# Optimization experiments

Measured on AMD Instinct MI355X. Metric: run time of the kernel, lower is better.

## Reference

```python
import jax, jax.numpy as jnp
import numpy as np

E = 2048        # embed_dim
H = 16          # num_heads
HKV = 4         # num_heads_kv (GQA)
D = 128         # head_dim
DCONV = 4       # causal depthwise conv width
ROT_DIM = 128   # rotary_emb_dim (= head_dim, full rotation)
ROT_BASE = 10000.0
QKV_DIM = D * (H + 2 * HKV)  # 3072
B, S = 2, 2048


def setup_inputs() -> dict:
    key = jax.random.key(0)
    ks = jax.random.split(key, 7)
    return {
        "x": jax.random.normal(ks[0], (B, S, E), jnp.float32),
        "W_in": jax.random.normal(ks[1], (E, QKV_DIM), jnp.float32) * 0.02,
        "b_in": jax.random.normal(ks[2], (QKV_DIM,), jnp.float32) * 0.02,
        "conv_w": jax.random.normal(ks[3], (QKV_DIM, DCONV), jnp.float32) * 0.1,
        "conv_b": jax.random.normal(ks[4], (QKV_DIM,), jnp.float32) * 0.02,
        "W_out": jax.random.normal(ks[5], (E, E), jnp.float32) * 0.02,
        "b_out": jax.random.normal(ks[6], (E,), jnp.float32) * 0.02,
    }


def _rotary_cos_sin(seqlen, dtype):
    # flash_attn RotaryEmbedding: inv_freq over even indices
    inv_freq = 1.0 / (ROT_BASE ** (np.arange(0, ROT_DIM, 2, dtype=np.float32) / ROT_DIM))
    t = np.arange(seqlen, dtype=np.float32)
    freqs = np.outer(t, inv_freq)                      # [S, ROT_DIM/2]
    return jnp.asarray(np.cos(freqs), dtype), jnp.asarray(np.sin(freqs), dtype)


def _apply_rotary(xh, cos, sin):
    # non-interleaved: rotate halves of the first ROT_DIM dims. xh: [B,S,h,D]
    x1 = xh[..., : ROT_DIM // 2]
    x2 = xh[..., ROT_DIM // 2 : ROT_DIM]
    c = cos[None, :, None, :]
    s = sin[None, :, None, :]
    rot = jnp.concatenate([x1 * c - x2 * s, x2 * c + x1 * s], axis=-1)
    return jnp.concatenate([rot, xh[..., ROT_DIM:]], axis=-1)


def _forward(x, W_in, b_in, conv_w, conv_b, W_out, b_out):
    b, s, _ = x.shape
    qkv = x @ W_in + b_in                              # [B,S,QKV_DIM]

    # causal depthwise conv1d (kernel DCONV, left-pad DCONV-1, trim right)
    xp = jnp.pad(qkv, ((0, 0), (DCONV - 1, 0), (0, 0)))
    conv = conv_b
    for k in range(DCONV):
        conv = conv + xp[:, k : k + s, :] * conv_w[:, k]
    qkv = conv                                         # [B,S,QKV_DIM]

    q, kv = jnp.split(qkv, [H * D], axis=-1)
    q = q.reshape(b, s, H, D)
    kv = kv.reshape(b, s, 2, HKV, D)
    k, v = kv[:, :, 0], kv[:, :, 1]                    # [B,S,HKV,D]

    cos, sin = _rotary_cos_sin(s, x.dtype)
    q = _apply_rotary(q, cos, sin)
    k = _apply_rotary(k, cos, sin)

    # GQA: repeat kv heads
    rep = H // HKV
    k = jnp.repeat(k, rep, axis=2)                     # [B,S,H,D]
    v = jnp.repeat(v, rep, axis=2)

    scale = 1.0 / np.sqrt(D)
    scores = jnp.einsum("bqhd,bkhd->bhqk", q, k) * scale
    causal = jnp.tril(jnp.ones((s, s), bool))
    scores = jnp.where(causal[None, None], scores, jnp.finfo(scores.dtype).min)
    probs = jax.nn.softmax(scores, axis=-1)
    ctx = jnp.einsum("bhqk,bkhd->bqhd", probs, v)      # [B,S,H,D]

    return ctx.reshape(b, s, H * D) @ W_out + b_out    # [B,S,E]


def reference(x, W_in, b_in, conv_w, conv_b, W_out, b_out):
    return _forward(x, W_in, b_in, conv_w, conv_b, W_out, b_out)
```

## Files before the change

kernel.cpp:

```cpp
#include <hip/hip_runtime.h>
#include <hip/hip_bf16.h>

#define B_    2
#define S_    2048
#define E_    2048
#define H_    16
#define HKV_  4
#define D_    128
#define QKV_  3072

#define LOG2E  1.4426950408889634f
#define SCALE  0.08838834764831845f
#define SL     0.127517431f
#define DEFER_THR 62.7f

typedef __attribute__((ext_vector_type(8))) short short8;
typedef __attribute__((ext_vector_type(4))) float floatx4;

typedef __attribute__((address_space(1))) const unsigned int gu32;
typedef __attribute__((address_space(3))) unsigned int lu32;

__device__ __forceinline__ void load_lds16(const unsigned short* g, unsigned short* l) {
    __builtin_amdgcn_global_load_lds((gu32*)g, (lu32*)l, 16, 0, 0);
}

__device__ __forceinline__ float b2f(unsigned short u) {
    union { unsigned int i; float f; } v; v.i = ((unsigned int)u) << 16; return v.f;
}
__device__ __forceinline__ unsigned short f2b(float f) {
    union { float f; unsigned int i; } v; v.f = f;
    unsigned int r = v.i + 0x7FFFu + ((v.i >> 16) & 1u);
    return (unsigned short)(r >> 16);
}
__device__ __forceinline__ unsigned int fbits(float f) {
    union { float f; unsigned int i; } v; v.f = f; return v.i;
}
__device__ __forceinline__ float bits2f(unsigned int i) {
    union { unsigned int i; float f; } v; v.i = i; return v.f;
}

template<int N> __device__ __forceinline__ void waitcnt_vm() {
    static_assert(N >= 0 && N <= 16, "vmcnt out of range");
    if constexpr (N == 0) asm volatile("s_waitcnt vmcnt(0)" ::: "memory");
    else if constexpr (N == 4) asm volatile("s_waitcnt vmcnt(4)" ::: "memory");
    else if constexpr (N == 6) asm volatile("s_waitcnt vmcnt(6)" ::: "memory");
    else if constexpr (N == 8) asm volatile("s_waitcnt vmcnt(8)" ::: "memory");
    else asm volatile("s_waitcnt vmcnt(2)" ::: "memory");
}

__global__ __launch_bounds__(256) void cvt_f32_bf16(
    const float* __restrict__ src, unsigned short* __restrict__ dst, int n)
{
    int i = (blockIdx.x * 256 + threadIdx.x) * 4;
    if (i + 3 < n) {
        float4 v = *(const float4*)&src[i];
        ushort4 o;
        o.x = f2b(v.x); o.y = f2b(v.y); o.z = f2b(v.z); o.w = f2b(v.w);
        *(ushort4*)&dst[i] = o;
    }
}

__global__ __launch_bounds__(256) void transpose_f32_bf16(
    const float* __restrict__ src, unsigned short* __restrict__ dst,
    int R, int C)
{
    __shared__ unsigned short tile[32][33];
    const int c0 = blockIdx.x * 32, r0 = blockIdx.y * 32;
    const int tx = threadIdx.x, ty = threadIdx.y;
    #pragma unroll
    for (int i = 0; i < 4; i++)
        tile[ty + 8 * i][tx] = f2b(src[(size_t)(r0 + ty + 8 * i) * C + c0 + tx]);
    __syncthreads();
    #pragma unroll
    for (int i = 0; i < 4; i++)
        dst[(size_t)(c0 + ty + 8 * i) * R + r0 + tx] = tile[tx][ty + 8 * i];
}

__global__ __launch_bounds__(256) void transpose_bf16(
    const unsigned short* __restrict__ src, unsigned short* __restrict__ dst,
    int R, int C)
{
    __shared__ unsigned short tile[32][33];
    const size_t boff = (size_t)blockIdx.z * R * C;
    src += boff; dst += boff;
    const int c0 = blockIdx.x * 32, r0 = blockIdx.y * 32;
    const int tx = threadIdx.x, ty = threadIdx.y;
    #pragma unroll
    for (int i = 0; i < 4; i++)
        tile[ty + 8 * i][tx] = src[(size_t)(r0 + ty + 8 * i) * C + c0 + tx];
    __syncthreads();
    #pragma unroll
    for (int i = 0; i < 4; i++)
        dst[(size_t)(c0 + ty + 8 * i) * R + r0 + tx] = tile[tx][ty + 8 * i];
}

template<int WR, int QR, int LX>
__device__ __forceinline__ void stage_unit8(
    const unsigned short* __restrict__ G, unsigned short* ls,
    int uu, int g0, int K, int k0, int wave, int lane)
{
    #pragma unroll
    for (int l = 0; l < LX; ++l) {
        const int c    = wave * LX + l;
        const int rr   = c / (QR / 8);
        const int row0 = rr * WR + uu * QR + (c % (QR / 8)) * 8;
        const int srow = row0 + (lane >> 3);
        const int sg   = (lane & 7) ^ (lane >> 3);
        load_lds16(&G[(size_t)(g0 + srow) * K + k0 + sg * 8], &ls[row0 * 64]);
    }
}

template<int BN, int WM, int WN, int OUTF32>
__global__ __launch_bounds__(512, 2) void gemm8(
    const unsigned short* __restrict__ A, const unsigned short* __restrict__ Bt,
    const float* __restrict__ bias, void* __restrict__ Cv,
    int M, int N, int K)
{
    constexpr int BM   = 256;
    constexpr int WMR  = BM / WM, WNR = BN / WN;
    constexpr int QMR  = WMR / 2, QNR = WNR / 2;
    constexpr int FM   = QMR / 16, FN = QNR / 16;
    constexpr int LA   = BM / 128, LB = BN / 128;
    constexpr int TILE = (BM + BN) * 64;

    __shared__ unsigned short lds[2 * TILE];

    const int tid  = threadIdx.x;
    const int wave = tid >> 6, lane = tid & 63;
    const int ln   = lane & 15, kq = lane >> 4;
    const int wm   = wave / WN, wn = wave % WN;

    const int nwg = gridDim.x;
    const int wg  = (blockIdx.x & 7) * (nwg >> 3) + (blockIdx.x >> 3);
    const int nbn = N / BN;
    const int m0  = (wg / nbn) * BM, n0 = (wg % nbn) * BN;

    floatx4 acc[2 * FM][2 * FN];
    #pragma unroll
    for (int i = 0; i < 2 * FM; ++i)
        #pragma unroll
        for (int j = 0; j < 2 * FN; ++j) {
            acc[i][j][0] = 0.f; acc[i][j][1] = 0.f;
            acc[i][j][2] = 0.f; acc[i][j][3] = 0.f;
        }

    stage_unit8<WMR, QMR, LA>(A,  &lds[0],       0, m0, K, 0, wave, lane);
    stage_unit8<WNR, QNR, LB>(Bt, &lds[BM * 64], 0, n0, K, 0, wave, lane);
    stage_unit8<WNR, QNR, LB>(Bt, &lds[BM * 64], 1, n0, K, 0, wave, lane);
    stage_unit8<WMR, QMR, LA>(A,  &lds[0],       1, m0, K, 0, wave, lane);
    waitcnt_vm<4>();
    __builtin_amdgcn_s_barrier();

    const int NT = K >> 6;
    int cur = 0;

    for (int t = 0; t < NT - 1; ++t) {
        const unsigned short* Asp = &lds[cur * TILE];
        const unsigned short* Bsp = Asp + BM * 64;
        unsigned short* Ssp = &lds[(cur ^ 1) * TILE];
        const int k1 = (t + 1) << 6;
        #pragma unroll
        for (int p = 0; p < 4; ++p) {
            const int qm = p >> 1, qn = p & 1;
            short8 af[2][FM], bg[2][FN];
            #pragma unroll
            for (int ks = 0; ks < 2; ++ks) {
                #pragma unroll
                for (int i = 0; i < FM; ++i)
                    af[ks][i] = *(const short8*)&Asp[(wm * WMR + qm * QMR + i * 16 + ln) * 64
                                                     + (((ks * 4 + kq) ^ (ln & 7)) * 8)];
                #pragma unroll
                for (int j = 0; j < FN; ++j)
                    bg[ks][j] = *(const short8*)&Bsp[(wn * WNR + qn * QNR + j * 16 + ln) * 64
                                                     + (((ks * 4 + kq) ^ (ln & 7)) * 8)];
            }
            if (p == 0)      stage_unit8<WMR, QMR, LA>(A,  Ssp,           0, m0, K, k1, wave, lane);
            else if (p == 1) stage_unit8<WNR, QNR, LB>(Bt, Ssp + BM * 64, 0, n0, K, k1, wave, lane);
            else if (p == 2) stage_unit8<WNR, QNR, LB>(Bt, Ssp + BM * 64, 1, n0, K, k1, wave, lane);
            else             stage_unit8<WMR, QMR, LA>(A,  Ssp,           1, m0, K, k1, wave, lane);
            __builtin_amdgcn_s_barrier();
            __builtin_amdgcn_s_setprio(1);
            #pragma unroll
            for (int ks = 0; ks < 2; ++ks)
                #pragma unroll
                for (int i = 0; i < FM; ++i)
                    #pragma unroll
                    for (int j = 0; j < FN; ++j)
                        acc[qm * FM + i][qn * FN + j] = __builtin_amdgcn_mfma_f32_16x16x32_bf16(
                            af[ks][i], bg[ks][j], acc[qm * FM + i][qn * FN + j], 0, 0, 0);
            __builtin_amdgcn_s_setprio(0);
            if (p == 0)      waitcnt_vm<2 * LA>();
            else if (p == 1) waitcnt_vm<LA + LB>();
            else if (p == 2) waitcnt_vm<LA + 2 * LB>();
            else             waitcnt_vm<LA + LB>();
            __builtin_amdgcn_s_barrier();
        }
        cur ^= 1;
    }

    asm volatile("s_waitcnt vmcnt(0)" ::: "memory");
    __builtin_amdgcn_s_barrier();
    {
        const unsigned short* Asp = &lds[cur * TILE];
        const unsigned short* Bsp = Asp + BM * 64;
        #pragma unroll
        for (int p = 0; p < 4; ++p) {
            const int qm = p >> 1, qn = p & 1;
            short8 af[2][FM], bg[2][FN];
            #pragma unroll
            for (int ks = 0; ks < 2; ++ks) {
                #pragma unroll
                for (int i = 0; i < FM; ++i)
                    af[ks][i] = *(const short8*)&Asp[(wm * WMR + qm * QMR + i * 16 + ln) * 64
                                                     + (((ks * 4 + kq) ^ (ln & 7)) * 8)];
                #pragma unroll
                for (int j = 0; j < FN; ++j)
                    bg[ks][j] = *(const short8*)&Bsp[(wn * WNR + qn * QNR + j * 16 + ln) * 64
                                                     + (((ks * 4 + kq) ^ (ln & 7)) * 8)];
            }
            __builtin_amdgcn_s_setprio(1);
            #pragma unroll
            for (int ks = 0; ks < 2; ++ks)
                #pragma unroll
                for (int i = 0; i < FM; ++i)
                    #pragma unroll
                    for (int j = 0; j < FN; ++j)
                        acc[qm * FM + i][qn * FN + j] = __builtin_amdgcn_mfma_f32_16x16x32_bf16(
                            af[ks][i], bg[ks][j], acc[qm * FM + i][qn * FN + j], 0, 0, 0);
            __builtin_amdgcn_s_setprio(0);
        }
    }

    #pragma unroll
    for (int nj = 0; nj < 2 * FN; ++nj) {
        const int col = n0 + wn * WNR + nj * 16 + ln;
        const float bv = bias[col];
        #pragma unroll
        for (int mi = 0; mi < 2 * FM; ++mi) {
            const int rowb = m0 + wm * WMR + mi * 16 + kq * 4;
            #pragma unroll
            for (int r = 0; r < 4; ++r) {
                const float val = acc[mi][nj][r] + bv;
                if (OUTF32) ((float*)Cv)[(size_t)(rowb + r) * N + col] = val;
                else ((unsigned short*)Cv)[(size_t)(rowb + r) * N + col] = f2b(val);
            }
        }
    }
}

__device__ __forceinline__ float conv_at(
    const unsigned short* __restrict__ qb, const float* __restrict__ cw,
    const float* __restrict__ cb, int s, int c)
{
    float acc = cb[c];
    const float* w = cw + c * 4;
    #pragma unroll
    for (int t = 0; t < 4; t++) {
        int sp = s - 3 + t;
        if (sp >= 0) acc += b2f(qb[(size_t)sp * QKV_ + c]) * w[t];
    }
    return acc;
}

__global__ __launch_bounds__(256) void conv_rot(
    const unsigned short* __restrict__ qkv, const float* __restrict__ cw,
    const float* __restrict__ cb, unsigned short* __restrict__ qo,
    unsigned short* __restrict__ ko, unsigned short* __restrict__ vo)
{
    const int bs = blockIdx.x;
    const int b = bs >> 11, s = bs & 2047;
    const unsigned short* qb = qkv + (size_t)b * S_ * QKV_;

    for (int it = threadIdx.x; it < 1792; it += 256) {
        if (it < 1280) {
            const int isq = it < 1024;
            const int rel = isq ? it : it - 1024;
            const int head = rel >> 6, d = rel & 63;
            const int c1 = (isq ? head * 128 : 2048 + head * 128) + d;
            float x1 = conv_at(qb, cw, cb, s, c1);
            float x2 = conv_at(qb, cw, cb, s, c1 + 64);
            float inv = exp2f((float)d * -0.2076205059304601f);
            float ang = (float)s * inv;
            float sn, cs;
            __sincosf(ang, &sn, &cs);
            float r1 = x1 * cs - x2 * sn;
            float r2 = x2 * cs + x1 * sn;
            unsigned short* dst = isq
                ? qo + ((size_t)(b * H_   + head) * S_ + s) * D_
                : ko + ((size_t)(b * HKV_ + head) * S_ + s) * D_;
            dst[d]      = f2b(r1);
            dst[d + 64] = f2b(r2);
        } else {
            const int idx = it - 1280;
            const int g = idx >> 7, d = idx & 127;
            float vv = conv_at(qb, cw, cb, s, 2560 + idx);
            vo[((size_t)(b * HKV_ + g) * S_ + s) * D_ + d] = f2b(vv);
        }
    }
}

__global__ __launch_bounds__(256, 4) void attn(
    const unsigned short* __restrict__ q, const unsigned short* __restrict__ k,
    const unsigned short* __restrict__ vT, unsigned short* __restrict__ ctx)
{
    __shared__ unsigned short Ks[64 * 128];
    __shared__ unsigned short Vs[128 * 64];
    __shared__ unsigned short Ps[4][16][64];

    const int h = blockIdx.x, qy = blockIdx.y, b = blockIdx.z, g = h >> 2;
    const int qt = (qy < 16) ? (31 - qy) : (qy - 16);
    const int tid = threadIdx.x, wave = tid >> 6, lane = tid & 63;
    const int ln = lane & 15, kq = lane >> 4;

    const unsigned short* qh = q  + (size_t)(b * H_   + h) * S_ * D_;
    const unsigned short* kh = k  + (size_t)(b * HKV_ + g) * S_ * D_;
    const unsigned short* vh = vT + (size_t)(b * HKV_ + g) * D_ * S_;

    const int rK = (lane >> 4);
    const int pK = lane & 15;
    const int rV = (lane >> 3);
    const int pV = lane & 7;

    const int qrow0 = qt * 64 + wave * 16;

    short8 qf[4];
    #pragma unroll
    for (int f = 0; f < 4; f++)
        qf[f] = *(const short8*)&qh[(size_t)(qrow0 + ln) * D_ + f * 32 + kq * 8];

    floatx4 o[8];
    #pragma unroll
    for (int i = 0; i < 8; i++) { o[i][0] = 0.f; o[i][1] = 0.f; o[i][2] = 0.f; o[i][3] = 0.f; }
    float mr = -INFINITY, lr = 0.f;

    for (int kt = 0; kt <= qt; kt++) {
        __syncthreads();
        #pragma unroll
        for (int c = 0; c < 4; c++) {
            const int chunk = wave * 4 + c;
            int r  = chunk * 4 + rK;
            int gc = pK ^ (r & 15);
            load_lds16(&kh[(size_t)(kt * 64 + r) * D_ + gc * 8], &Ks[chunk * 512]);
            int rv = chunk * 8 + rV;
            int gv = pV ^ (rv & 7);
            load_lds16(&vh[(size_t)rv * S_ + kt * 64 + gv * 8], &Vs[chunk * 512]);
        }
        __syncthreads();

        floatx4 scv[4];
        #pragma unroll
        for (int nb = 0; nb < 4; nb++) { scv[nb][0]=0.f; scv[nb][1]=0.f; scv[nb][2]=0.f; scv[nb][3]=0.f; }
        __builtin_amdgcn_s_setprio(1);
        #pragma unroll
        for (int ks = 0; ks < 4; ks++) {
            #pragma unroll
            for (int nb = 0; nb < 4; nb++) {
                short8 kf = *(const short8*)&Ks[(nb * 16 + ln) * 128 + (((ks * 4 + kq) ^ ln) * 8)];
                scv[nb] = __builtin_amdgcn_mfma_f32_16x16x32_bf16(kf, qf[ks], scv[nb], 0, 0, 0);
            }
        }
        __builtin_amdgcn_s_setprio(0);

        if (kt == qt) {
            const int qloc = wave * 16 + ln;
            #pragma unroll
            for (int nb = 0; nb < 4; nb++)
                #pragma unroll
                for (int r = 0; r < 4; r++)
                    if (nb * 16 + kq * 4 + r > qloc) scv[nb][r] = -INFINITY;
        }

        float mx = -INFINITY;
        #pragma unroll
        for (int nb = 0; nb < 4; nb++) {
            float a0 = fmaxf(scv[nb][0], scv[nb][1]);
            float a1 = fmaxf(scv[nb][2], scv[nb][3]);
            mx = fmaxf(mx, fmaxf(a0, a1));
        }
        mx = fmaxf(mx, __shfl_xor(mx, 16));
        mx = fmaxf(mx, __shfl_xor(mx, 32));

        float mt = mr, al = 1.0f;
        if (!__all(mx - mr <= DEFER_THR)) {
            mt = fmaxf(mr, mx);
            al = exp2f((mr - mt) * SL);
            mr = mt;
            float alr[4];
            #pragma unroll
            for (int r = 0; r < 4; r++) alr[r] = __shfl(al, kq * 4 + r);
            #pragma unroll
            for (int dn = 0; dn < 8; dn++)
                #pragma unroll
                for (int r = 0; r < 4; r++) o[dn][r] *= alr[r];
        }

        float rs = 0.f;
        #pragma unroll
        for (int nb = 0; nb < 4; nb++) {
            const int gct = 2 * nb + (kq >> 1);
            const int pbase = ((gct ^ (ln & 7)) << 3) + ((kq & 1) << 2);
            #pragma unroll
            for (int rr = 0; rr < 2; rr++) {
                unsigned int u0 = fbits(exp2f((scv[nb][2 * rr]     - mt) * SL));
                unsigned int u1 = fbits(exp2f((scv[nb][2 * rr + 1] - mt) * SL));
                rs += bits2f(u0 & 0xFFFF0000u) + bits2f(u1 & 0xFFFF0000u);
                *(unsigned int*)&Ps[wave][ln][pbase + 2 * rr] =
                    (u0 >> 16) | (u1 & 0xFFFF0000u);
            }
        }
        rs += __shfl_xor(rs, 16);
        rs += __shfl_xor(rs, 32);
        lr = lr * al + rs;

        short8 pa0 = *(const short8*)&Ps[wave][ln][(kq ^ (ln & 7)) << 3];
        short8 pa1 = *(const short8*)&Ps[wave][ln][((4 + kq) ^ (ln & 7)) << 3];
        __builtin_amdgcn_s_setprio(1);
        #pragma unroll
        for (int dn = 0; dn < 8; dn++) {
            short8 b0 = *(const short8*)&Vs[(dn * 16 + ln) * 64 + ((kq ^ (ln & 7)) * 8)];
            o[dn] = __builtin_amdgcn_mfma_f32_16x16x32_bf16(pa0, b0, o[dn], 0, 0, 0);
            short8 b1 = *(const short8*)&Vs[(dn * 16 + ln) * 64 + (((4 + kq) ^ (ln & 7)) * 8)];
            o[dn] = __builtin_amdgcn_mfma_f32_16x16x32_bf16(pa1, b1, o[dn], 0, 0, 0);
        }
        __builtin_amdgcn_s_setprio(0);
    }

    float lrr[4];
    #pragma unroll
    for (int r = 0; r < 4; r++) lrr[r] = 1.0f / __shfl(lr, kq * 4 + r);
    #pragma unroll
    for (int r = 0; r < 4; r++) {
        size_t rowoff = (size_t)(b * S_ + qt * 64 + wave * 16 + kq * 4 + r) * (H_ * D_) + h * D_;
        #pragma unroll
        for (int dn = 0; dn < 8; dn++)
            ctx[rowoff + dn * 16 + ln] = f2b(o[dn][r] * lrr[r]);
    }
}

extern "C" void kernel_launch(void* const* d_in, const int* in_sizes, int n_in,
                              void* d_out, int out_size, void* d_ws, size_t ws_size,
                              hipStream_t stream)
{
    const float* x     = (const float*)d_in[0];
    const float* W_in  = (const float*)d_in[1];
    const float* b_in  = (const float*)d_in[2];
    const float* cw    = (const float*)d_in[3];
    const float* cb    = (const float*)d_in[4];
    const float* W_out = (const float*)d_in[5];
    const float* b_out = (const float*)d_in[6];
    float* out = (float*)d_out;
    char* ws = (char*)d_ws;

    const size_t MB = 1024 * 1024;
    unsigned short* WtIn  = (unsigned short*)(ws);
    unsigned short* WtOut = (unsigned short*)(ws + 12 * MB);
    unsigned short* x16   = (unsigned short*)(ws + 20 * MB);
    unsigned short* qkv   = (unsigned short*)(ws + 36 * MB);
    unsigned short* qa    = (unsigned short*)(ws + 60 * MB);
    unsigned short* ka    = (unsigned short*)(ws + 76 * MB);
    unsigned short* va    = (unsigned short*)(ws + 80 * MB);
    unsigned short* vTa   = (unsigned short*)(ws + 84 * MB);
    unsigned short* ctx   = (unsigned short*)(ws + 20 * MB);

    dim3 tb(32, 8);
    hipLaunchKernelGGL(cvt_f32_bf16, dim3(8192), dim3(256), 0, stream, x, x16, 8388608);
    hipLaunchKernelGGL(transpose_f32_bf16, dim3(96, 64), tb, 0, stream, W_in,  WtIn,  2048, 3072);
    hipLaunchKernelGGL(transpose_f32_bf16, dim3(64, 64), tb, 0, stream, W_out, WtOut, 2048, 2048);
    hipLaunchKernelGGL((gemm8<256, 2, 4, 0>), dim3(192), dim3(512), 0, stream,
                       x16, WtIn, b_in, (void*)qkv, 4096, 3072, 2048);
    hipLaunchKernelGGL(conv_rot, dim3(4096), dim3(256), 0, stream, qkv, cw, cb, qa, ka, va);
    hipLaunchKernelGGL(transpose_bf16, dim3(4, 64, 8), tb, 0, stream, va, vTa, 2048, 128);
    hipLaunchKernelGGL(attn, dim3(16, 32, 2), dim3(256), 0, stream, qa, ka, vTa, ctx);
    hipLaunchKernelGGL((gemm8<128, 4, 2, 1>), dim3(256), dim3(512), 0, stream,
                       ctx, WtOut, b_out, (void*)out, 4096, 2048, 2048);
}
```

Baseline: 367.0 us.

## Double-buffer K/V tiles in attention and use 128-row query blocks with 8 waves

The attention kernel now processes 128 query rows per block with 512 threads (8 waves), so each K/V tile is shared across twice as many query rows. K/V tiles are double-buffered in LDS, with the next tile prefetched via global_load_lds while the current one is computed, using waitcnt plus raw barriers instead of syncthreads. Load balancing changes from pairing short and long query tiles to reversing the tile order on batch 1. Waves whose rows lie entirely above the diagonal skip the tile, but they still wait at the barriers. The cost is more LDS per block, which can lower occupancy under launch_bounds(512,4).

```diff
diff --git a/kernel.cpp b/kernel.cpp
--- a/kernel.cpp
+++ b/kernel.cpp
@@ -299,16 +299,16 @@
     }
 }
 
-__global__ __launch_bounds__(256, 4) void attn(
+__global__ __launch_bounds__(512, 4) void attn(
     const unsigned short* __restrict__ q, const unsigned short* __restrict__ k,
     const unsigned short* __restrict__ vT, unsigned short* __restrict__ ctx)
 {
-    __shared__ unsigned short Ks[64 * 128];
-    __shared__ unsigned short Vs[128 * 64];
-    __shared__ unsigned short Ps[4][16][64];
+    __shared__ unsigned short Ks[2][64 * 128];
+    __shared__ unsigned short Vs[2][128 * 64];
+    __shared__ unsigned short Ps[8][16][64];
 
     const int h = blockIdx.x, qy = blockIdx.y, b = blockIdx.z, g = h >> 2;
-    const int qt = (qy < 16) ? (31 - qy) : (qy - 16);
+    const int qt = b ? (15 - qy) : qy;
     const int tid = threadIdx.x, wave = tid >> 6, lane = tid & 63;
     const int ln = lane & 15, kq = lane >> 4;
 
@@ -321,7 +321,7 @@
     const int rV = (lane >> 3);
     const int pV = lane & 7;
 
-    const int qrow0 = qt * 64 + wave * 16;
+    const int qrow0 = qt * 128 + wave * 16;
 
     short8 qf[4];
     #pragma unroll
@@ -333,96 +333,122 @@
     for (int i = 0; i < 8; i++) { o[i][0] = 0.f; o[i][1] = 0.f; o[i][2] = 0.f; o[i][3] = 0.f; }
     float mr = -INFINITY, lr = 0.f;
 
-    for (int kt = 0; kt <= qt; kt++) {
-        __syncthreads();
+    const int KT = 2 * qt + 2;
+
+    {
         #pragma unroll
-        for (int c = 0; c < 4; c++) {
-            const int chunk = wave * 4 + c;
+        for (int c = 0; c < 2; c++) {
+            const int chunk = wave * 2 + c;
             int r  = chunk * 4 + rK;
             int gc = pK ^ (r & 15);
-            load_lds16(&kh[(size_t)(kt * 64 + r) * D_ + gc * 8], &Ks[chunk * 512]);
+            load_lds16(&kh[(size_t)r * D_ + gc * 8], &Ks[0][chunk * 512]);
             int rv = chunk * 8 + rV;
             int gv = pV ^ (rv & 7);
-            load_lds16(&vh[(size_t)rv * S_ + kt * 64 + gv * 8], &Vs[chunk * 512]);
-        }
-        __syncthreads();
-
-        floatx4 scv[4];
-        #pragma unroll
-        for (int nb = 0; nb < 4; nb++) { scv[nb][0]=0.f; scv[nb][1]=0.f; scv[nb][2]=0.f; scv[nb][3]=0.f; }
-        __builtin_amdgcn_s_setprio(1);
-        #pragma unroll
-        for (int ks = 0; ks < 4; ks++) {
+            load_lds16(&vh[(size_t)rv * S_ + gv * 8], &Vs[0][chunk * 512]);
+        }
+    }
+
+    for (int kt = 0; kt < KT; kt++) {
+        const int buf = kt & 1;
+        if (kt + 1 < KT) {
+            #pragma unroll
+            for (int c = 0; c < 2; c++) {
+                const int chunk = wave * 2 + c;
+                int r  = chunk * 4 + rK;
+                int gc = pK ^ (r & 15);
+                load_lds16(&kh[(size_t)((kt + 1) * 64 + r) * D_ + gc * 8],
+                           &Ks[buf ^ 1][chunk * 512]);
+                int rv = chunk * 8 + rV;
+                int gv = pV ^ (rv & 7);
+                load_lds16(&vh[(size_t)rv * S_ + (kt + 1) * 64 + gv * 8],
+                           &Vs[buf ^ 1][chunk * 512]);
+            }
+            waitcnt_vm<4>();
+        } else {
+            waitcnt_vm<0>();
+        }
+        __builtin_amdgcn_s_barrier();
+
+        if (kt * 64 <= qrow0 + 15) {
+            floatx4 scv[4];
+            #pragma unroll
+            for (int nb = 0; nb < 4; nb++) { scv[nb][0]=0.f; scv[nb][1]=0.f; scv[nb][2]=0.f; scv[nb][3]=0.f; }
+            __builtin_amdgcn_s_setprio(1);
+            #pragma unroll
+            for (int ks = 0; ks < 4; ks++) {
+                #pragma unroll
+                for (int nb = 0; nb < 4; nb++) {
+                    short8 kf = *(const short8*)&Ks[buf][(nb * 16 + ln) * 128 + (((ks * 4 + kq) ^ ln) * 8)];
+                    scv[nb] = __builtin_amdgcn_mfma_f32_16x16x32_bf16(kf, qf[ks], scv[nb], 0, 0, 0);
+                }
+            }
+            __builtin_amdgcn_s_setprio(0);
+
+            if (kt * 64 + 63 > qrow0) {
+                const int qi = qrow0 + ln;
+                #pragma unroll
+                for (int nb = 0; nb < 4; nb++)
+                    #pragma unroll
+                    for (int r = 0; r < 4; r++)
+                        if (kt * 64 + nb * 16 + kq * 4 + r > qi) scv[nb][r] = -INFINITY;
+            }
+
+            float mx = -INFINITY;
             #pragma unroll
             for (int nb = 0; nb < 4; nb++) {
-                short8 kf = *(const short8*)&Ks[(nb * 16 + ln) * 128 + (((ks * 4 + kq) ^ ln) * 8)];
-                scv[nb] = __builtin_amdgcn_mfma_f32_16x16x32_bf16(kf, qf[ks], scv[nb], 0, 0, 0);
-            }
-        }
-        __builtin_amdgcn_s_setprio(0);
-
-        if (kt == qt) {
-            const int qloc = wave * 16 + ln;
-            #pragma unroll
-            for (int nb = 0; nb < 4; nb++)
-                #pragma unroll
-                for (int r = 0; r < 4; r++)
-                    if (nb * 16 + kq * 4 + r > qloc) scv[nb][r] = -INFINITY;
-        }
-
-        float mx = -INFINITY;
-        #pragma unroll
-        for (int nb = 0; nb < 4; nb++) {
-            float a0 = fmaxf(scv[nb][0], scv[nb][1]);
-            float a1 = fmaxf(scv[nb][2], scv[nb][3]);
-            mx = fmaxf(mx, fmaxf(a0, a1));
-        }
-        mx = fmaxf(mx, __shfl_xor(mx, 16));
-        mx = fmaxf(mx, __shfl_xor(mx, 32));
-
-        float mt = mr, al = 1.0f;
-        if (!__all(mx - mr <= DEFER_THR)) {
-            mt = fmaxf(mr, mx);
-            al = exp2f((mr - mt) * SL);
-            mr = mt;
-            float alr[4];
-            #pragma unroll
-            for (int r = 0; r < 4; r++) alr[r] = __shfl(al, kq * 4 + r);
-            #pragma unroll
-            for (int dn = 0; dn < 8; dn++)
-                #pragma unroll
-                for (int r = 0; r < 4; r++) o[dn][r] *= alr[r];
-        }
-
-        float rs = 0.f;
-        #pragma unroll
-        for (int nb = 0; nb < 4; nb++) {
-            const int gct = 2 * nb + (kq >> 1);
-            const int pbase = ((gct ^ (ln & 7)) << 3) + ((kq & 1) << 2);
-            #pragma unroll
-            for (int rr = 0; rr < 2; rr++) {
-                unsigned int u0 = fbits(exp2f((scv[nb][2 * rr]     - mt) * SL));
-                unsigned int u1 = fbits(exp2f((scv[nb][2 * rr + 1] - mt) * SL));
-                rs += bits2f(u0 & 0xFFFF0000u) + bits2f(u1 & 0xFFFF0000u);
-                *(unsigned int*)&Ps[wave][ln][pbase + 2 * rr] =
-                    (u0 >> 16) | (u1 & 0xFFFF0000u);
-            }
-        }
-        rs += __shfl_xor(rs, 16);
-        rs += __shfl_xor(rs, 32);
-        lr = lr * al + rs;
-
-        short8 pa0 = *(const short8*)&Ps[wave][ln][(kq ^ (ln & 7)) << 3];
-        short8 pa1 = *(const short8*)&Ps[wave][ln][((4 + kq) ^ (ln & 7)) << 3];
-        __builtin_amdgcn_s_setprio(1);
-        #pragma unroll
-        for (int dn = 0; dn < 8; dn++) {
-            short8 b0 = *(const short8*)&Vs[(dn * 16 + ln) * 64 + ((kq ^ (ln & 7)) * 8)];
-            o[dn] = __builtin_amdgcn_mfma_f32_16x16x32_bf16(pa0, b0, o[dn], 0, 0, 0);
-            short8 b1 = *(const short8*)&Vs[(dn * 16 + ln) * 64 + (((4 + kq) ^ (ln & 7)) * 8)];
-            o[dn] = __builtin_amdgcn_mfma_f32_16x16x32_bf16(pa1, b1, o[dn], 0, 0, 0);
-        }
-        __builtin_amdgcn_s_setprio(0);
+                float a0 = fmaxf(scv[nb][0], scv[nb][1]);
+                float a1 = fmaxf(scv[nb][2], scv[nb][3]);
+                mx = fmaxf(mx, fmaxf(a0, a1));
+            }
+            mx = fmaxf(mx, __shfl_xor(mx, 16));
+            mx = fmaxf(mx, __shfl_xor(mx, 32));
+
+            float mt = mr, al = 1.0f;
+            if (!__all(mx - mr <= DEFER_THR)) {
+                mt = fmaxf(mr, mx);
+                al = exp2f((mr - mt) * SL);
+                mr = mt;
+                float alr[4];
+                #pragma unroll
+                for (int r = 0; r < 4; r++) alr[r] = __shfl(al, kq * 4 + r);
+                #pragma unroll
+                for (int dn = 0; dn < 8; dn++)
+                    #pragma unroll
+                    for (int r = 0; r < 4; r++) o[dn][r] *= alr[r];
+            }
+
+            float rs = 0.f;
+            #pragma unroll
+            for (int nb = 0; nb < 4; nb++) {
+                const int gct = 2 * nb + (kq >> 1);
+                const int pbase = ((gct ^ (ln & 7)) << 3) + ((kq & 1) << 2);
+                #pragma unroll
+                for (int rr = 0; rr < 2; rr++) {
+                    unsigned int u0 = fbits(exp2f((scv[nb][2 * rr]     - mt) * SL));
+                    unsigned int u1 = fbits(exp2f((scv[nb][2 * rr + 1] - mt) * SL));
+                    rs += bits2f(u0 & 0xFFFF0000u) + bits2f(u1 & 0xFFFF0000u);
+                    *(unsigned int*)&Ps[wave][ln][pbase + 2 * rr] =
+                        (u0 >> 16) | (u1 & 0xFFFF0000u);
+                }
+            }
+            rs += __shfl_xor(rs, 16);
+            rs += __shfl_xor(rs, 32);
+            lr = lr * al + rs;
+
+            short8 pa0 = *(const short8*)&Ps[wave][ln][(kq ^ (ln & 7)) << 3];
+            short8 pa1 = *(const short8*)&Ps[wave][ln][((4 + kq) ^ (ln & 7)) << 3];
+            __builtin_amdgcn_s_setprio(1);
+            #pragma unroll
+            for (int dn = 0; dn < 8; dn++) {
+                short8 b0 = *(const short8*)&Vs[buf][(dn * 16 + ln) * 64 + ((kq ^ (ln & 7)) * 8)];
+                o[dn] = __builtin_amdgcn_mfma_f32_16x16x32_bf16(pa0, b0, o[dn], 0, 0, 0);
+                short8 b1 = *(const short8*)&Vs[buf][(dn * 16 + ln) * 64 + (((4 + kq) ^ (ln & 7)) * 8)];
+                o[dn] = __builtin_amdgcn_mfma_f32_16x16x32_bf16(pa1, b1, o[dn], 0, 0, 0);
+            }
+            __builtin_amdgcn_s_setprio(0);
+        }
+
+        __builtin_amdgcn_s_barrier();
     }
 
     float lrr[4];
@@ -430,7 +456,7 @@
     for (int r = 0; r < 4; r++) lrr[r] = 1.0f / __shfl(lr, kq * 4 + r);
     #pragma unroll
     for (int r = 0; r < 4; r++) {
-        size_t rowoff = (size_t)(b * S_ + qt * 64 + wave * 16 + kq * 4 + r) * (H_ * D_) + h * D_;
+        size_t rowoff = (size_t)(b * S_ + qrow0 + kq * 4 + r) * (H_ * D_) + h * D_;
         #pragma unroll
         for (int dn = 0; dn < 8; dn++)
             ctx[rowoff + dn * 16 + ln] = f2b(o[dn][r] * lrr[r]);
@@ -470,7 +496,7 @@
                        x16, WtIn, b_in, (void*)qkv, 4096, 3072, 2048);
     hipLaunchKernelGGL(conv_rot, dim3(4096), dim3(256), 0, stream, qkv, cw, cb, qa, ka, va);
     hipLaunchKernelGGL(transpose_bf16, dim3(4, 64, 8), tb, 0, stream, va, vTa, 2048, 128);
-    hipLaunchKernelGGL(attn, dim3(16, 32, 2), dim3(256), 0, stream, qa, ka, vTa, ctx);
+    hipLaunchKernelGGL(attn, dim3(16, 16, 2), dim3(512), 0, stream, qa, ka, vTa, ctx);
     hipLaunchKernelGGL((gemm8<128, 4, 2, 1>), dim3(256), dim3(512), 0, stream,
                        ctx, WtOut, b_out, (void*)out, 4096, 2048, 2048);
 }
```

New measurement: 363.0 us. No clear change (-1.1%).
